# Performance work log

Measured on AMD Instinct MI355X. Metric: run time of the kernel, lower is better.

## Reference

```python
import jax, jax.numpy as jnp
import numpy as np

E = 512   # embed_dim
H = 16    # num_heads
D = E // H  # head_dim = 32
L = 2048  # target (query) length
S = 2048  # source (stored pattern) length
N = 4     # batch
LN_EPS = 1e-5


def setup_inputs() -> dict:
    key = jax.random.key(0)
    ks = jax.random.split(key, 8)
    inv_sqrt_e = 1.0 / np.sqrt(E).astype(np.float32)
    return {
        "query": jax.random.normal(ks[0], (L, N, E), jnp.float32),
        "key_in": jax.random.normal(ks[1], (S, N, E), jnp.float32),
        "value": jax.random.normal(ks[2], (S, N, E), jnp.float32),
        "scaling": jax.random.uniform(ks[3], (H,), jnp.float32),  # per-head beta
        "in_proj_weight": jax.random.normal(ks[4], (3 * E, E), jnp.float32) * inv_sqrt_e,
        "in_proj_bias": jnp.zeros((3 * E,), jnp.float32),
        "p_norm_weight": jnp.ones((D,), jnp.float32),
        "p_norm_bias": jnp.zeros((D,), jnp.float32),
        "out_proj_weight": jax.random.normal(ks[5], (E, E), jnp.float32) * inv_sqrt_e,
        "out_proj_bias": jnp.zeros((E,), jnp.float32),
    }


def reference(query, key_in, value, scaling, in_proj_weight, in_proj_bias,
              p_norm_weight, p_norm_bias, out_proj_weight, out_proj_bias):
    Lq, Nb, Ed = query.shape
    Sk = key_in.shape[0]
    # split packed in-projection (torch Linear convention: y = x @ W^T + b)
    wq, wk, wv = jnp.split(in_proj_weight, 3, axis=0)
    bq, bk, bv = jnp.split(in_proj_bias, 3, axis=0)
    q = jnp.einsum('lne,fe->lnf', query, wq) + bq
    k = jnp.einsum('sne,fe->snf', key_in, wk) + bk
    v = jnp.einsum('sne,fe->snf', value, wv) + bv
    # (len, N, H*D) -> (N, H, len, D)
    q = q.reshape(Lq, Nb, H, D).transpose(1, 2, 0, 3)
    k = k.reshape(Sk, Nb, H, D).transpose(1, 2, 0, 3)
    v = v.reshape(Sk, Nb, H, D).transpose(1, 2, 0, 3)

    def pattern_norm(x):
        # affine LayerNorm over the association (head) dimension D
        mu = jnp.mean(x, axis=-1, keepdims=True)
        var = jnp.mean(jnp.square(x - mu), axis=-1, keepdims=True)
        return (x - mu) * jax.lax.rsqrt(var + LN_EPS) * p_norm_weight + p_norm_bias

    k = pattern_norm(k)
    v = pattern_norm(v)

    beta = scaling.reshape(1, H, 1, 1)  # per-head inverse-temperature
    scores = jnp.einsum('nhld,nhsd->nhls', q * beta, k)  # [N,H,L,S]
    attn = jax.nn.softmax(scores, axis=-1)  # single Hopfield update (update_steps_max=0)
    out = jnp.einsum('nhls,nhsd->nhld', attn, v)  # [N,H,L,D]
    out = out.transpose(2, 0, 1, 3).reshape(Lq, Nb, H * D)
    out = jnp.einsum('lnf,of->lno', out, out_proj_weight) + out_proj_bias
    return out  # (L, N, E)
```

## Files before the change

kernel.cpp:

```cpp
#include <hip/hip_runtime.h>
#include <cstdint>

#define LN_EPS 1e-5f

typedef _Float16 f16;
typedef _Float16 half4_t __attribute__((ext_vector_type(4)));
typedef _Float16 half8_t __attribute__((ext_vector_type(8)));
typedef __fp16 fp16v2 __attribute__((ext_vector_type(2)));
typedef float f32x4 __attribute__((ext_vector_type(4)));

__device__ __forceinline__ void gl_lds16(const void* g, void* l) {
    __builtin_amdgcn_global_load_lds(
        (__attribute__((address_space(1))) void*)(uintptr_t)g,
        (__attribute__((address_space(3))) void*)(uint32_t)(uintptr_t)l,
        16, 0, 0);
}

__device__ __forceinline__ half4_t pack4(float a, float b, float c, float d) {
    fp16v2 lo = __builtin_amdgcn_cvt_pkrtz(a, b);
    fp16v2 hi = __builtin_amdgcn_cvt_pkrtz(c, d);
    half4_t r;
    r[0] = (f16)lo[0]; r[1] = (f16)lo[1]; r[2] = (f16)hi[0]; r[3] = (f16)hi[1];
    return r;
}

__global__ void k_cast(const float* __restrict__ W1f, const float* __restrict__ W2f,
                       const float* __restrict__ Xq, const float* __restrict__ Xk,
                       const float* __restrict__ Xv,
                       f16* __restrict__ W1h, f16* __restrict__ W2h,
                       f16* __restrict__ Xh) {
    int t0 = blockIdx.x * blockDim.x + threadIdx.x;
    #pragma unroll
    for (int rep = 0; rep < 4; ++rep) {
        int t = t0 + rep * 851968;
        const float4* src;
        half4_t* dst;
        int idx;
        if (t < 196608)      { src = (const float4*)W1f; dst = (half4_t*)W1h; idx = t; }
        else if (t < 262144) { src = (const float4*)W2f; dst = (half4_t*)W2h; idx = t - 196608; }
        else {
            int u = t - 262144;
            int s = u >> 20;
            idx = u & 1048575;
            src = (s == 0) ? (const float4*)Xq : ((s == 1) ? (const float4*)Xk : (const float4*)Xv);
            dst = (half4_t*)(Xh + (size_t)s * 4194304);
        }
        float4 v = src[idx];
        dst[idx] = pack4(v.x, v.y, v.z, v.w);
    }
}

__global__ __launch_bounds__(256) void k_inproj(
    const f16* __restrict__ Xh, const f16* __restrict__ W1,
    const float* __restrict__ bias, const float* __restrict__ scaling,
    const float* __restrict__ pnw, const float* __restrict__ pnb,
    f16* __restrict__ Qg, f16* __restrict__ Kg, f16* __restrict__ Vtg)
{
    __shared__ __align__(16) char pool[49152];

    const int tid = threadIdx.x;
    const int bid = blockIdx.x;
    const int jj = bid >> 3;
    const int m0 = ((bid & 7) * 8 + (jj & 7)) * 128;
    const int f0 = (jj >> 3) * 128;
    const int sec = f0 >> 9;
    const f16* X = Xh + (size_t)sec * 4194304;
    f16* Ob = (sec == 0) ? Qg : Kg;

    const int wid = tid >> 6, ln = tid & 63, l15 = ln & 15, quad = ln >> 4;
    const int wm = wid >> 1, wn = wid & 1;
    const int srow = ln >> 2, sco = (ln & 3) * 8;

    f32x4 z4 = {0.f, 0.f, 0.f, 0.f};
    f32x4 acc[4][4];
    #pragma unroll
    for (int i = 0; i < 4; ++i)
        #pragma unroll
        for (int j = 0; j < 4; ++j) acc[i][j] = z4;

    auto issue = [&](int kt, int slot) {
        const int k0 = kt * 32;
        f16* As = (f16*)(pool + slot * 16384);
        f16* Bs = (f16*)(pool + slot * 16384 + 8192);
        #pragma unroll
        for (int i = 0; i < 2; ++i) {
            int row = wid * 32 + i * 16 + srow;
            gl_lds16(W1 + (size_t)(f0 + row) * 512 + k0 + sco,
                     Bs + (wid * 32 + i * 16) * 32);
            gl_lds16(X + (size_t)(m0 + row) * 512 + k0 + sco,
                     As + (wid * 32 + i * 16) * 32);
        }
    };
    issue(0, 0);
    issue(1, 1);

    int slot = 0;
    for (int kt = 0; kt < 16; ++kt) {
        if (kt < 15) asm volatile("s_waitcnt vmcnt(4)" ::: "memory");
        else         asm volatile("s_waitcnt vmcnt(0)" ::: "memory");
        __builtin_amdgcn_s_barrier();

        if (kt < 14) {
            int nb = slot + 2; if (nb >= 3) nb -= 3;
            issue(kt + 2, nb);
        }

        const f16* As = (const f16*)(pool + slot * 16384);
        const f16* Bs = (const f16*)(pool + slot * 16384 + 8192);
        half8_t a[4], b[4];
        #pragma unroll
        for (int i = 0; i < 4; ++i)
            a[i] = *(const half8_t*)(As + (wm * 64 + i * 16 + l15) * 32 + quad * 8);
        #pragma unroll
        for (int j = 0; j < 4; ++j)
            b[j] = *(const half8_t*)(Bs + (wn * 64 + j * 16 + l15) * 32 + quad * 8);
        __builtin_amdgcn_s_setprio(1);
        #pragma unroll
        for (int i = 0; i < 4; ++i)
            #pragma unroll
            for (int j = 0; j < 4; ++j)
                acc[i][j] = __builtin_amdgcn_mfma_f32_16x16x32_f16(b[j], a[i], acc[i][j], 0, 0, 0);
        __builtin_amdgcn_s_setprio(0);

        slot = slot + 1; if (slot == 3) slot = 0;
    }

    __syncthreads();
    f16* Ep = (f16*)pool;

    float sQa = 0.f, sQb = 0.f;
    float4 wA, wB, bA, bB;
    if (sec == 0) {
        int hbase = ((f0 & 511) >> 5) + wn * 2;
        sQa = scaling[hbase] * 1.44269504f;
        sQb = scaling[hbase + 1] * 1.44269504f;
    } else {
        wA = *(const float4*)(pnw + quad * 4);
        wB = *(const float4*)(pnw + 16 + quad * 4);
        bA = *(const float4*)(pnb + quad * 4);
        bB = *(const float4*)(pnb + 16 + quad * 4);
    }
    float4 bias4[4];
    #pragma unroll
    for (int j = 0; j < 4; ++j)
        bias4[j] = *(const float4*)(bias + f0 + wn * 64 + j * 16 + quad * 4);

    #pragma unroll
    for (int i = 0; i < 4; ++i) {
        float x[4][4];
        #pragma unroll
        for (int j = 0; j < 4; ++j) {
            x[j][0] = acc[i][j][0] + bias4[j].x;
            x[j][1] = acc[i][j][1] + bias4[j].y;
            x[j][2] = acc[i][j][2] + bias4[j].z;
            x[j][3] = acc[i][j][3] + bias4[j].w;
        }
        if (sec == 0) {
            #pragma unroll
            for (int j = 0; j < 4; ++j) {
                float sc = (j < 2) ? sQa : sQb;
                #pragma unroll
                for (int r = 0; r < 4; ++r) x[j][r] *= sc;
            }
        } else {
            #pragma unroll
            for (int hp = 0; hp < 2; ++hp) {
                float s1 = 0.f, s2 = 0.f;
                #pragma unroll
                for (int jq = 0; jq < 2; ++jq) {
                    int j = hp * 2 + jq;
                    #pragma unroll
                    for (int r = 0; r < 4; ++r) { s1 += x[j][r]; s2 += x[j][r] * x[j][r]; }
                }
                s1 += __shfl_xor(s1, 16); s1 += __shfl_xor(s1, 32);
                s2 += __shfl_xor(s2, 16); s2 += __shfl_xor(s2, 32);
                float mu = s1 * (1.f / 32.f);
                float rs = rsqrtf(s2 * (1.f / 32.f) - mu * mu + LN_EPS);
                #pragma unroll
                for (int jq = 0; jq < 2; ++jq) {
                    int j = hp * 2 + jq;
                    const float4& wv = (j & 1) ? wB : wA;
                    const float4& bv = (j & 1) ? bB : bA;
                    x[j][0] = (x[j][0] - mu) * rs * wv.x + bv.x;
                    x[j][1] = (x[j][1] - mu) * rs * wv.y + bv.y;
                    x[j][2] = (x[j][2] - mu) * rs * wv.z + bv.z;
                    x[j][3] = (x[j][3] - mu) * rs * wv.w + bv.w;
                }
            }
        }
        int mloc = wm * 64 + i * 16 + l15;
        int key = (mloc >> 2) & 7;
        #pragma unroll
        for (int j = 0; j < 4; ++j) {
            int floc0 = wn * 64 + j * 16 + quad * 4;
            *(half4_t*)(Ep + mloc * 128 + (floc0 ^ (key << 3))) =
                pack4(x[j][0], x[j][1], x[j][2], x[j][3]);
        }
    }
    __syncthreads();

    if (sec < 2) {
        int fgrp = (tid >> 6) * 4 + quad;
        int fs = (f0 & 511) + fgrp * 8;
        int hh = fs >> 5, cc = (fs >> 3) & 3;
        #pragma unroll
        for (int it = 0; it < 8; ++it) {
            int nb = it & 3, lblk = it >> 2;
            int L = lblk * 16 + l15;
            int mloc = nb + 4 * L;
            half8_t v = *(const half8_t*)(Ep + mloc * 128 + ((fgrp ^ (L & 7)) << 3));
            int gg = nb * 16 + hh;
            size_t l = (size_t)(m0 >> 2) + L;
            *(half8_t*)(Ob + (size_t)gg * 65536 + (size_t)cc * 16384 + l * 8) = v;
        }
    } else {
        int seg = m0 >> 8;
        int csb = ((m0 >> 7) & 1) * 4;
        int hbase = (f0 & 511) >> 5;
        #pragma unroll
        for (int p = 0; p < 2; ++p) {
            int idx = tid * 2 + p;
            int g16 = idx >> 5, d = idx & 31;
            int nb = g16 >> 2, hhl = g16 & 3;
            int floc = hhl * 32 + d;
            size_t obase = (size_t)((nb * 16 + hbase + hhl) * 32 + seg) * 2048 + d * 64;
            #pragma unroll
            for (int cq = 0; cq < 4; ++cq) {
                half8_t hv;
                #pragma unroll
                for (int es = 0; es < 8; ++es) {
                    int mloc = nb + 4 * (cq * 8 + es);
                    hv[es] = Ep[mloc * 128 + (floc ^ (es << 3))];
                }
                int csx = (csb + cq) ^ (d & 7);
                *(half8_t*)(Vtg + obase + csx * 8) = hv;
            }
        }
    }
}

__global__ __launch_bounds__(256, 4) void k_flash(
    const f16* __restrict__ Qg, const f16* __restrict__ Kg,
    const f16* __restrict__ Vtg, f16* __restrict__ Og)
{
    __shared__ __align__(16) char smem[40960];

    const int tid = threadIdx.x, wid = tid >> 6, ln = tid & 63;
    const int l15 = ln & 15, quad = ln >> 4, l8 = ln & 7;
    char* Pw = smem + 24576 + wid * 4096;
    const int g = blockIdx.x, h = g & 15, n = g >> 4;
    const int q0 = blockIdx.y * 128;

    half8_t aq[2];
    #pragma unroll
    for (int i = 0; i < 2; ++i)
        aq[i] = *(const half8_t*)(Qg + (size_t)g * 65536 + (size_t)quad * 16384 +
                                  (size_t)(q0 + wid * 32 + i * 16 + l15) * 8);

    const f16* kp = Kg + (size_t)g * 65536 + (size_t)wid * 16384;
    const f16* vp = Vtg + (size_t)(g * 32) * 2048 + wid * 512;
    gl_lds16(kp + (size_t)ln * 8, smem + wid * 1024);
    gl_lds16(vp + (size_t)ln * 8, smem + 12288 + wid * 1024);
    gl_lds16(kp + 512 + (size_t)ln * 8, smem + 4096 + wid * 1024);
    gl_lds16(vp + 2048 + (size_t)ln * 8, smem + 12288 + 4096 + wid * 1024);
    kp += 1024;
    vp += 4096;

    half8_t onesf;
    {
        f16 o = (l15 == 0) ? (f16)1.0f : (f16)0.0f;
        #pragma unroll
        for (int j = 0; j < 8; ++j) onesf[j] = o;
    }

    f32x4 z4 = {0.f, 0.f, 0.f, 0.f};
    f32x4 accO[2][2], accSum[2];
    accO[0][0] = z4; accO[0][1] = z4; accO[1][0] = z4; accO[1][1] = z4;
    accSum[0] = z4; accSum[1] = z4;
    float m_i[2] = {-1e30f, -1e30f};

    const char* K0s = smem;          const char* V0s = smem + 12288;
    const char* K1s = smem + 4096;   const char* V1s = smem + 16384;
    const char* K2s = smem + 8192;   const char* V2s = smem + 20480;

    auto body = [&](const char* Kl, const char* Vt, char* Kn, char* Vn, int st) {
        if (st < 31) asm volatile("s_waitcnt vmcnt(2)" ::: "memory");
        else         asm volatile("s_waitcnt vmcnt(0)" ::: "memory");
        __builtin_amdgcn_s_barrier();

        if (st < 30) {
            gl_lds16(kp + (size_t)ln * 8, Kn + wid * 1024);
            gl_lds16(vp + (size_t)ln * 8, Vn + wid * 1024);
            kp += 512;
            vp += 2048;
        }

        half8_t ak[4];
        #pragma unroll
        for (int mt = 0; mt < 4; ++mt)
            ak[mt] = *(const half8_t*)(Kl + quad * 1024 + (mt * 16 + l15) * 16);
        f32x4 accS[2][4];
        __builtin_amdgcn_s_setprio(1);
        #pragma unroll
        for (int i = 0; i < 2; ++i)
            #pragma unroll
            for (int mt = 0; mt < 4; ++mt)
                accS[i][mt] = __builtin_amdgcn_mfma_f32_16x16x32_f16(ak[mt], aq[i], z4, 0, 0, 0);
        __builtin_amdgcn_s_setprio(0);

        float mn[2];
        bool up = false;
        #pragma unroll
        for (int i = 0; i < 2; ++i) {
            float xm = fmaxf(fmaxf(accS[i][0][0], accS[i][0][1]), accS[i][0][2]);
            xm = fmaxf(fmaxf(xm, accS[i][0][3]), accS[i][1][0]);
            xm = fmaxf(fmaxf(xm, accS[i][1][1]), accS[i][1][2]);
            xm = fmaxf(fmaxf(xm, accS[i][1][3]), accS[i][2][0]);
            xm = fmaxf(fmaxf(xm, accS[i][2][1]), accS[i][2][2]);
            xm = fmaxf(fmaxf(xm, accS[i][2][3]), accS[i][3][0]);
            xm = fmaxf(fmaxf(xm, accS[i][3][1]), accS[i][3][2]);
            xm = fmaxf(xm, accS[i][3][3]);
            xm = fmaxf(xm, __shfl_xor(xm, 16));
            xm = fmaxf(xm, __shfl_xor(xm, 32));
            up = up || (xm > m_i[i] + 8.f);
            mn[i] = fmaxf(m_i[i], xm);
        }
        if (__ballot(up)) {
            #pragma unroll
            for (int i = 0; i < 2; ++i) {
                float alpha = __builtin_amdgcn_exp2f(m_i[i] - mn[i]);
                #pragma unroll
                for (int dt = 0; dt < 2; ++dt)
                    #pragma unroll
                    for (int r = 0; r < 4; ++r) accO[i][dt][r] *= alpha;
                #pragma unroll
                for (int r = 0; r < 4; ++r) accSum[i][r] *= alpha;
                m_i[i] = mn[i];
            }
        }

        #pragma unroll
        for (int i = 0; i < 2; ++i) {
            #pragma unroll
            for (int mt = 0; mt < 4; ++mt) {
                float p0 = __builtin_amdgcn_exp2f(accS[i][mt][0] - m_i[i]);
                float p1 = __builtin_amdgcn_exp2f(accS[i][mt][1] - m_i[i]);
                float p2 = __builtin_amdgcn_exp2f(accS[i][mt][2] - m_i[i]);
                float p3 = __builtin_amdgcn_exp2f(accS[i][mt][3] - m_i[i]);
                int ch = (mt * 2 + (quad >> 1)) ^ l8;
                *(half4_t*)(Pw + (i * 16 + l15) * 128 + ch * 16 + (quad & 1) * 8) =
                    pack4(p0, p1, p2, p3);
            }
        }

        #pragma unroll
        for (int kt = 0; kt < 2; ++kt) {
            half8_t av[2], bp[2];
            #pragma unroll
            for (int dt = 0; dt < 2; ++dt) {
                int d = dt * 16 + l15;
                int cp = (kt * 4 + quad) ^ (l15 & 7);
                av[dt] = *(const half8_t*)(Vt + d * 128 + cp * 16);
            }
            #pragma unroll
            for (int i = 0; i < 2; ++i)
                bp[i] = *(const half8_t*)(Pw + (i * 16 + l15) * 128 +
                                          (((kt * 4 + quad) ^ l8) * 16));
            __builtin_amdgcn_s_setprio(1);
            #pragma unroll
            for (int i = 0; i < 2; ++i) {
                #pragma unroll
                for (int dt = 0; dt < 2; ++dt)
                    accO[i][dt] = __builtin_amdgcn_mfma_f32_16x16x32_f16(av[dt], bp[i], accO[i][dt], 0, 0, 0);
                accSum[i] = __builtin_amdgcn_mfma_f32_16x16x32_f16(onesf, bp[i], accSum[i], 0, 0, 0);
            }
            __builtin_amdgcn_s_setprio(0);
        }
    };

    #pragma unroll 1
    for (int tt = 0; tt < 10; ++tt) {
        body(K0s, V0s, (char*)K2s, (char*)V2s, tt * 3);
        body(K1s, V1s, (char*)K0s, (char*)V0s, tt * 3 + 1);
        body(K2s, V2s, (char*)K1s, (char*)V1s, tt * 3 + 2);
    }
    body(K0s, V0s, (char*)K2s, (char*)V2s, 30);
    body(K1s, V1s, (char*)K0s, (char*)V0s, 31);

    #pragma unroll
    for (int i = 0; i < 2; ++i) {
        float li = __shfl(accSum[i][0], l15);
        float inv = 1.f / li;
        #pragma unroll
        for (int dt = 0; dt < 2; ++dt)
            *(half4_t*)(Pw + (i * 16 + l15) * 80 + (dt * 16 + quad * 4) * 2) =
                pack4(accO[i][dt][0] * inv, accO[i][dt][1] * inv,
                      accO[i][dt][2] * inv, accO[i][dt][3] * inv);
    }
    int q2 = ln >> 1, hf = ln & 1;
    half8_t o0 = *(const half8_t*)(Pw + q2 * 80 + hf * 32);
    half8_t o1 = *(const half8_t*)(Pw + q2 * 80 + hf * 32 + 16);
    size_t rowe = ((size_t)(n * 2048 + q0 + wid * 32 + q2)) * 512 + h * 32 + hf * 16;
    *(half8_t*)(Og + rowe) = o0;
    *(half8_t*)(Og + rowe + 8) = o1;
}

__global__ __launch_bounds__(256) void k_outproj(
    const f16* __restrict__ A, const f16* __restrict__ W2,
    const float* __restrict__ bias, float* __restrict__ Out)
{
    __shared__ __align__(16) char pool[36864];

    const int tid = threadIdx.x;
    const int m0 = blockIdx.x * 64;
    const int f0 = blockIdx.y * 128;
    const int wid = tid >> 6, ln = tid & 63, l15 = ln & 15, quad = ln >> 4;
    const int wm = wid >> 1, wn = wid & 1;
    const int srow = ln >> 2, sco = (ln & 3) * 8;

    f32x4 z4 = {0.f, 0.f, 0.f, 0.f};
    f32x4 acc[2][4];
    #pragma unroll
    for (int i = 0; i < 2; ++i)
        #pragma unroll
        for (int j = 0; j < 4; ++j) acc[i][j] = z4;

    auto issue = [&](int kt, int slot) {
        const int k0 = kt * 32;
        f16* As = (f16*)(pool + slot * 12288);
        f16* Bs = (f16*)(pool + slot * 12288 + 4096);
        int arow = wid * 16 + srow;
        gl_lds16(A + (size_t)(m0 + arow) * 512 + k0 + sco,
                 As + wid * 512);
        #pragma unroll
        for (int i = 0; i < 2; ++i) {
            int brow = wid * 32 + i * 16 + srow;
            gl_lds16(W2 + (size_t)(f0 + brow) * 512 + k0 + sco,
                     Bs + (wid * 32 + i * 16) * 32);
        }
    };
    issue(0, 0);
    issue(1, 1);

    int slot = 0;
    for (int kt = 0; kt < 16; ++kt) {
        if (kt < 15) asm volatile("s_waitcnt vmcnt(3)" ::: "memory");
        else         asm volatile("s_waitcnt vmcnt(0)" ::: "memory");
        __builtin_amdgcn_s_barrier();

        if (kt < 14) {
            int nb = slot + 2; if (nb >= 3) nb -= 3;
            issue(kt + 2, nb);
        }

        const f16* As = (const f16*)(pool + slot * 12288);
        const f16* Bs = (const f16*)(pool + slot * 12288 + 4096);
        half8_t a[2], b[4];
        #pragma unroll
        for (int i = 0; i < 2; ++i)
            a[i] = *(const half8_t*)(As + (wm * 32 + i * 16 + l15) * 32 + quad * 8);
        #pragma unroll
        for (int j = 0; j < 4; ++j)
            b[j] = *(const half8_t*)(Bs + (wn * 64 + j * 16 + l15) * 32 + quad * 8);
        __builtin_amdgcn_s_setprio(1);
        #pragma unroll
        for (int i = 0; i < 2; ++i)
            #pragma unroll
            for (int j = 0; j < 4; ++j)
                acc[i][j] = __builtin_amdgcn_mfma_f32_16x16x32_f16(b[j], a[i], acc[i][j], 0, 0, 0);
        __builtin_amdgcn_s_setprio(0);

        slot = slot + 1; if (slot == 3) slot = 0;
    }

    __syncthreads();
    float* Ef = (float*)pool;

    #pragma unroll
    for (int j = 0; j < 4; ++j) {
        int floc0 = wn * 64 + j * 16 + quad * 4;
        float4 bs4 = *(const float4*)(bias + f0 + floc0);
        #pragma unroll
        for (int i = 0; i < 2; ++i) {
            int mloc = wm * 32 + i * 16 + l15;
            float4 o;
            o.x = acc[i][j][0] + bs4.x;
            o.y = acc[i][j][1] + bs4.y;
            o.z = acc[i][j][2] + bs4.z;
            o.w = acc[i][j][3] + bs4.w;
            *(float4*)(Ef + mloc * 132 + floc0) = o;
        }
    }
    __syncthreads();

    {
        int hw = tid >> 5, lane32 = tid & 31;
        #pragma unroll
        for (int it = 0; it < 8; ++it) {
            int row = it * 8 + hw;
            float4 v = *(const float4*)(Ef + row * 132 + lane32 * 4);
            int rm = m0 + row;
            int orow = (rm & 2047) * 4 + (rm >> 11);
            *(float4*)(Out + (size_t)orow * 512 + f0 + lane32 * 4) = v;
        }
    }
}

extern "C" void kernel_launch(void* const* d_in, const int* in_sizes, int n_in,
                              void* d_out, int out_size, void* d_ws, size_t ws_size,
                              hipStream_t stream) {
    const float* query   = (const float*)d_in[0];
    const float* key_in  = (const float*)d_in[1];
    const float* value   = (const float*)d_in[2];
    const float* scaling = (const float*)d_in[3];
    const float* ipw     = (const float*)d_in[4];
    const float* ipb     = (const float*)d_in[5];
    const float* pnw     = (const float*)d_in[6];
    const float* pnb     = (const float*)d_in[7];
    const float* opw     = (const float*)d_in[8];
    const float* opb     = (const float*)d_in[9];
    float* out = (float*)d_out;

    f16* Qg  = (f16*)d_ws;
    f16* Kg  = Qg + (size_t)4194304;
    f16* Vtg = Qg + (size_t)8388608;
    f16* W1  = Qg + (size_t)12582912;
    f16* W2  = Qg + (size_t)13369344;
    f16* Xh  = Qg + (size_t)13631488;
    f16* Og  = Xh;

    k_cast<<<3328, 256, 0, stream>>>(ipw, opw, query, key_in, value, W1, W2, Xh);
    k_inproj<<<768, 256, 0, stream>>>(Xh, W1, ipb, scaling, pnw, pnb, Qg, Kg, Vtg);
    k_flash<<<dim3(64, 16), 256, 0, stream>>>(Qg, Kg, Vtg, Og);
    k_outproj<<<dim3(128, 4), 256, 0, stream>>>(Og, W2, opb, out);
}
```

Baseline: 206.5 us.

## Software-pipeline QK^T one tile ahead of softmax and PV in attention loop

Restructures the attention main loop so the QK^T MFMA for the next key tile is issued before the softmax and PV work on the current tile's scores, with double-buffered score registers (S0/S1). A prologue computes the first tile's scores, and the loop is unrolled by six to alternate register sets. The vmcnt wait thresholds are adjusted to the new issue order. The aim is to overlap matrix-core latency with the exp and max VALU work, at the cost of more live accumulator registers and possible occupancy loss.

```diff
diff --git a/kernel.cpp b/kernel.cpp
--- a/kernel.cpp
+++ b/kernel.cpp
@@ -283,43 +283,61 @@
     const char* K1s = smem + 4096;   const char* V1s = smem + 16384;
     const char* K2s = smem + 8192;   const char* V2s = smem + 20480;
 
-    auto body = [&](const char* Kl, const char* Vt, char* Kn, char* Vn, int st) {
-        if (st < 31) asm volatile("s_waitcnt vmcnt(2)" ::: "memory");
-        else         asm volatile("s_waitcnt vmcnt(0)" ::: "memory");
+    f32x4 S0[2][4], S1[2][4];
+    asm volatile("s_waitcnt vmcnt(3)" ::: "memory");
+    __builtin_amdgcn_s_barrier();
+    {
+        half8_t ak[4];
+        #pragma unroll
+        for (int mt = 0; mt < 4; ++mt)
+            ak[mt] = *(const half8_t*)(K0s + quad * 1024 + (mt * 16 + l15) * 16);
+        #pragma unroll
+        for (int i = 0; i < 2; ++i)
+            #pragma unroll
+            for (int mt = 0; mt < 4; ++mt)
+                S0[i][mt] = __builtin_amdgcn_mfma_f32_16x16x32_f16(ak[mt], aq[i], z4, 0, 0, 0);
+    }
+
+    auto body = [&](f32x4 (&SC)[2][4], f32x4 (&SN)[2][4],
+                    const char* Vt, const char* Kn, char* Ki, char* Vi,
+                    bool doIssue, bool doQK, bool lastWait) {
+        if (!lastWait) asm volatile("s_waitcnt vmcnt(1)" ::: "memory");
+        else           asm volatile("s_waitcnt vmcnt(0)" ::: "memory");
         __builtin_amdgcn_s_barrier();
 
-        if (st < 30) {
-            gl_lds16(kp + (size_t)ln * 8, Kn + wid * 1024);
-            gl_lds16(vp + (size_t)ln * 8, Vn + wid * 1024);
+        if (doIssue) {
+            gl_lds16(kp + (size_t)ln * 8, Ki + wid * 1024);
+            gl_lds16(vp + (size_t)ln * 8, Vi + wid * 1024);
             kp += 512;
             vp += 2048;
         }
 
-        half8_t ak[4];
-        #pragma unroll
-        for (int mt = 0; mt < 4; ++mt)
-            ak[mt] = *(const half8_t*)(Kl + quad * 1024 + (mt * 16 + l15) * 16);
-        f32x4 accS[2][4];
-        __builtin_amdgcn_s_setprio(1);
-        #pragma unroll
-        for (int i = 0; i < 2; ++i)
+        if (doQK) {
+            half8_t ak[4];
             #pragma unroll
             for (int mt = 0; mt < 4; ++mt)
-                accS[i][mt] = __builtin_amdgcn_mfma_f32_16x16x32_f16(ak[mt], aq[i], z4, 0, 0, 0);
-        __builtin_amdgcn_s_setprio(0);
+                ak[mt] = *(const half8_t*)(Kn + quad * 1024 + (mt * 16 + l15) * 16);
+            __builtin_amdgcn_s_setprio(1);
+            #pragma unroll
+            for (int i = 0; i < 2; ++i)
+                #pragma unroll
+                for (int mt = 0; mt < 4; ++mt)
+                    SN[i][mt] = __builtin_amdgcn_mfma_f32_16x16x32_f16(ak[mt], aq[i], z4, 0, 0, 0);
+            __builtin_amdgcn_s_setprio(0);
+        }
 
         float mn[2];
         bool up = false;
         #pragma unroll
         for (int i = 0; i < 2; ++i) {
-            float xm = fmaxf(fmaxf(accS[i][0][0], accS[i][0][1]), accS[i][0][2]);
-            xm = fmaxf(fmaxf(xm, accS[i][0][3]), accS[i][1][0]);
-            xm = fmaxf(fmaxf(xm, accS[i][1][1]), accS[i][1][2]);
-            xm = fmaxf(fmaxf(xm, accS[i][1][3]), accS[i][2][0]);
-            xm = fmaxf(fmaxf(xm, accS[i][2][1]), accS[i][2][2]);
-            xm = fmaxf(fmaxf(xm, accS[i][2][3]), accS[i][3][0]);
-            xm = fmaxf(fmaxf(xm, accS[i][3][1]), accS[i][3][2]);
-            xm = fmaxf(xm, accS[i][3][3]);
+            float xm = fmaxf(fmaxf(SC[i][0][0], SC[i][0][1]), SC[i][0][2]);
+            xm = fmaxf(fmaxf(xm, SC[i][0][3]), SC[i][1][0]);
+            xm = fmaxf(fmaxf(xm, SC[i][1][1]), SC[i][1][2]);
+            xm = fmaxf(fmaxf(xm, SC[i][1][3]), SC[i][2][0]);
+            xm = fmaxf(fmaxf(xm, SC[i][2][1]), SC[i][2][2]);
+            xm = fmaxf(fmaxf(xm, SC[i][2][3]), SC[i][3][0]);
+            xm = fmaxf(fmaxf(xm, SC[i][3][1]), SC[i][3][2]);
+            xm = fmaxf(xm, SC[i][3][3]);
             xm = fmaxf(xm, __shfl_xor(xm, 16));
             xm = fmaxf(xm, __shfl_xor(xm, 32));
             up = up || (xm > m_i[i] + 8.f);
@@ -343,10 +361,10 @@
         for (int i = 0; i < 2; ++i) {
             #pragma unroll
             for (int mt = 0; mt < 4; ++mt) {
-                float p0 = __builtin_amdgcn_exp2f(accS[i][mt][0] - m_i[i]);
-                float p1 = __builtin_amdgcn_exp2f(accS[i][mt][1] - m_i[i]);
-                float p2 = __builtin_amdgcn_exp2f(accS[i][mt][2] - m_i[i]);
-                float p3 = __builtin_amdgcn_exp2f(accS[i][mt][3] - m_i[i]);
+                float p0 = __builtin_amdgcn_exp2f(SC[i][mt][0] - m_i[i]);
+                float p1 = __builtin_amdgcn_exp2f(SC[i][mt][1] - m_i[i]);
+                float p2 = __builtin_amdgcn_exp2f(SC[i][mt][2] - m_i[i]);
+                float p3 = __builtin_amdgcn_exp2f(SC[i][mt][3] - m_i[i]);
                 int ch = (mt * 2 + (quad >> 1)) ^ l8;
                 *(half4_t*)(Pw + (i * 16 + l15) * 128 + ch * 16 + (quad & 1) * 8) =
                     pack4(p0, p1, p2, p3);
@@ -379,13 +397,16 @@
     };
 
     #pragma unroll 1
-    for (int tt = 0; tt < 10; ++tt) {
-        body(K0s, V0s, (char*)K2s, (char*)V2s, tt * 3);
-        body(K1s, V1s, (char*)K0s, (char*)V0s, tt * 3 + 1);
-        body(K2s, V2s, (char*)K1s, (char*)V1s, tt * 3 + 2);
-    }
-    body(K0s, V0s, (char*)K2s, (char*)V2s, 30);
-    body(K1s, V1s, (char*)K0s, (char*)V0s, 31);
+    for (int tt = 0; tt < 5; ++tt) {
+        body(S0, S1, V0s, K1s, (char*)K2s, (char*)V2s, true, true, false);
+        body(S1, S0, V1s, K2s, (char*)K0s, (char*)V0s, true, true, false);
+        body(S0, S1, V2s, K0s, (char*)K1s, (char*)V1s, true, true, false);
+        body(S1, S0, V0s, K1s, (char*)K2s, (char*)V2s, true, true, false);
+        body(S0, S1, V1s, K2s, (char*)K0s, (char*)V0s, true, true, false);
+        body(S1, S0, V2s, K0s, (char*)K1s, (char*)V1s, true, true, false);
+    }
+    body(S0, S1, V0s, K1s, (char*)K2s, (char*)V2s, false, true, false);
+    body(S1, S0, V1s, K2s, (char*)K0s, (char*)V0s, false, false, true);
 
     #pragma unroll
     for (int i = 0; i < 2; ++i) {
```

Measured after the change: 226.6 us. 9.7% more time.
